# Kernel tuning notes

Hardware: AMD Instinct MI355X
Metric: run time of the kernel (lower is better)

Reference implementation:

```python
import jax, jax.numpy as jnp
import numpy as np

N_NODES = 100000
N_EDGES = 1600000
D = 128


def setup_inputs() -> dict:
    key = jax.random.key(0)
    ks = jax.random.split(key, 6)
    x = jax.random.normal(ks[0], (N_NODES, D), dtype=jnp.float32)
    src = jax.random.randint(ks[1], (N_EDGES,), 0, N_NODES, dtype=jnp.int32)
    dst = jax.random.randint(ks[2], (N_EDGES,), 0, N_NODES, dtype=jnp.int32)
    # Xavier-ish small weights
    W1 = jax.random.normal(ks[3], (D, D), dtype=jnp.float32) * 0.05
    W2 = jax.random.normal(ks[4], (D, D), dtype=jnp.float32) * 0.05
    b1 = jnp.zeros((D,), dtype=jnp.float32)
    b2 = jnp.zeros((D,), dtype=jnp.float32)
    prelu_a = jnp.full((1,), 0.25, dtype=jnp.float32)  # nn.PReLU default, shared across layers
    return {"x": x, "src": src, "dst": dst, "W1": W1, "b1": b1, "W2": W2, "b2": b2, "prelu_a": prelu_a}


def reference(x, src, dst, W1, b1, W2, b2, prelu_a):
    N = x.shape[0]
    # DGL GraphConv norm='left': scale source features by 1/clamp(out_degree, 1)
    deg = jax.ops.segment_sum(jnp.ones(src.shape, x.dtype), src, num_segments=N)
    inv_outdeg = (1.0 / jnp.maximum(deg, 1.0))[:, None]  # [N,1]

    def layer(h, W, b):
        h = h * inv_outdeg                                   # left-normalize sources
        agg = jax.ops.segment_sum(h[src], dst, num_segments=N)  # SpMM: sum messages at dst
        z = agg @ W + b                                      # dense transform (aggregate-first since in==out feats)
        return jnp.where(z >= 0, z, prelu_a * z)             # shared PReLU

    z = layer(x, W1, b1)
    z = layer(z, W2, b2)
    return z
```

## Files before the change

### kernel.cpp

```cpp
#include <hip/hip_runtime.h>

#define D 128
#define CAP 64
#define PADR 136

#define BSHIFT 9
#define NCH 512
#define BSTRIDE_LOG 14

typedef short short8 __attribute__((ext_vector_type(8)));
typedef float floatx4 __attribute__((ext_vector_type(4)));

static __device__ __forceinline__ unsigned short f2bf(float f) {
    unsigned int u = __float_as_uint(f);
    u += 0x7fffu + ((u >> 16) & 1u);
    return (unsigned short)(u >> 16);
}
static __device__ __forceinline__ unsigned int pack2bf(float a, float b) {
    return (unsigned int)f2bf(a) | ((unsigned int)f2bf(b) << 16);
}
static __device__ __forceinline__ int rd16(const unsigned int* __restrict__ pc, int v) {
    return (int)((pc[v >> 1] >> ((v & 1) * 16)) & 0xffffu);
}
static __device__ __forceinline__ void acc8(float* a, uint4 v) {
    a[0] += __uint_as_float(v.x << 16);  a[1] += __uint_as_float(v.x & 0xffff0000u);
    a[2] += __uint_as_float(v.y << 16);  a[3] += __uint_as_float(v.y & 0xffff0000u);
    a[4] += __uint_as_float(v.z << 16);  a[5] += __uint_as_float(v.z & 0xffff0000u);
    a[6] += __uint_as_float(v.w << 16);  a[7] += __uint_as_float(v.w & 0xffff0000u);
}

__global__ __launch_bounds__(512) void k_cnt(const int* __restrict__ src,
                                             const int* __restrict__ dst,
                                             unsigned int* __restrict__ gcd,
                                             unsigned int* __restrict__ gcs,
                                             int E, int cs, int nbuck) {
    __shared__ unsigned int hd[512], hs[512];
    int b = blockIdx.x, t = threadIdx.x;
    hd[t] = 0; hs[t] = 0;
    __syncthreads();
    int lo = b * cs, hi = lo + cs;
    if (hi > E) hi = E;
    for (int e = lo + t; e < hi; e += 512) {
        atomicAdd(&hd[(unsigned)dst[e] >> BSHIFT], 1u);
        atomicAdd(&hs[(unsigned)src[e] >> BSHIFT], 1u);
    }
    __syncthreads();
    for (int k = t; k < nbuck; k += 512) {
        gcd[(size_t)b * nbuck + k] = hd[k];
        gcs[(size_t)b * nbuck + k] = hs[k];
    }
}

__global__ __launch_bounds__(NCH) void k_pfx1(unsigned int* __restrict__ gcd,
                                              unsigned int* __restrict__ gcs,
                                              unsigned int* __restrict__ btd,
                                              unsigned int* __restrict__ bts, int nbuck) {
    __shared__ unsigned int sa[NCH], sb[NCH];
    int b = blockIdx.x, t = threadIdx.x;
    unsigned int* g  = (b < nbuck) ? gcd : gcs;
    unsigned int* bt = (b < nbuck) ? btd : bts;
    int k = (b < nbuck) ? b : (b - nbuck);
    unsigned int v = g[(size_t)t * nbuck + k];
    sa[t] = v;
    unsigned int* A = sa; unsigned int* B = sb;
    for (int off = 1; off < NCH; off <<= 1) {
        __syncthreads();
        B[t] = A[t] + ((t >= off) ? A[t - off] : 0u);
        unsigned int* tmp = A; A = B; B = tmp;
    }
    __syncthreads();
    unsigned int incl = A[t];
    g[(size_t)t * nbuck + k] = incl - v;
    if (t == NCH - 1) bt[k] = incl;
}

__global__ __launch_bounds__(512) void k_scat(const int* __restrict__ src, const int* __restrict__ dst,
                                              const unsigned int* __restrict__ gcd,
                                              const unsigned int* __restrict__ gcs,
                                              unsigned int* __restrict__ bdata,
                                              unsigned int* __restrict__ sdata,
                                              int E, int cs, int nbuck) {
    __shared__ unsigned int curd[512], curs[512];
    int b = blockIdx.x, t = threadIdx.x;
    for (int k = t; k < nbuck; k += 512) {
        curd[k] = ((unsigned int)k << BSTRIDE_LOG) + gcd[(size_t)b * nbuck + k];
        curs[k] = ((unsigned int)k << BSTRIDE_LOG) + gcs[(size_t)b * nbuck + k];
    }
    __syncthreads();
    int lo = b * cs, hi = lo + cs;
    if (hi > E) hi = E;
    for (int e = lo + t; e < hi; e += 512) {
        int s = src[e];
        int d = dst[e];
        unsigned int kd = (unsigned)d >> BSHIFT;
        unsigned int p = atomicAdd(&curd[kd], 1u);
        if (p < ((kd + 1u) << BSTRIDE_LOG))
            bdata[p] = ((unsigned int)(d & ((1 << BSHIFT) - 1)) << 17) | (unsigned int)s;
        unsigned int ks = (unsigned)s >> BSHIFT;
        unsigned int p2 = atomicAdd(&curs[ks], 1u);
        if (p2 < ((ks + 1u) << BSTRIDE_LOG))
            sdata[p2] = (unsigned int)(s & ((1 << BSHIFT) - 1));
    }
}

__global__ __launch_bounds__(256) void k_sdeg(const unsigned int* __restrict__ sdata,
                                              const unsigned int* __restrict__ bts,
                                              unsigned int* __restrict__ pcnt_out, int n) {
    __shared__ unsigned int cnt[1 << BSHIFT];
    int b = blockIdx.x;
    for (int k = threadIdx.x; k < (1 << BSHIFT); k += 256) cnt[k] = 0;
    __syncthreads();
    int lo = b << BSTRIDE_LOG;
    int c = (int)bts[b];
    if (c > (1 << BSTRIDE_LOG)) c = 1 << BSTRIDE_LOG;
    for (int i = threadIdx.x; i < c; i += 256)
        atomicAdd(&cnt[sdata[lo + i]], 1u);
    __syncthreads();
    int base = b << BSHIFT;
    for (int tt = threadIdx.x; tt < (1 << (BSHIFT - 1)); tt += 256) {
        int node0 = base + tt * 2;
        if (node0 < n) {
            unsigned int c0 = cnt[tt * 2];
            unsigned int c1 = cnt[tt * 2 + 1];
            pcnt_out[(base >> 1) + tt] = (c0 & 0xffffu) | (c1 << 16);
        }
    }
}

__global__ __launch_bounds__(256) void k_csrprep(
    const unsigned int* __restrict__ bdata, const unsigned int* __restrict__ btot,
    unsigned int* __restrict__ pcnt_in, int* __restrict__ esrc,
    const float* __restrict__ x, const unsigned int* __restrict__ pcnt_out,
    float* __restrict__ inv, uint2* __restrict__ xb2, int total4,
    const float* __restrict__ W1, const float* __restrict__ W2,
    unsigned short* __restrict__ WT1, unsigned short* __restrict__ WT2,
    uint4* __restrict__ z0, uint4* __restrict__ z1,
    int n, int nbuck) {
    __shared__ unsigned int lcnt[1 << BSHIFT];
    int b = blockIdx.x;

    if (b < nbuck) {
        int base = b << BSHIFT;
        for (int k = threadIdx.x; k < (1 << BSHIFT); k += 256) lcnt[k] = 0;
        __syncthreads();
        int lo = b << BSTRIDE_LOG;
        int cnt = (int)btot[b];
        if (cnt > (1 << BSTRIDE_LOG)) cnt = 1 << BSTRIDE_LOG;
        for (int i = threadIdx.x; i < cnt; i += 256) {
            unsigned int e = bdata[lo + i];
            int s = (int)(e & 0x1FFFFu);
            int dl = (int)(e >> 17);
            unsigned int p = atomicAdd(&lcnt[dl], 1u);
            if (p < CAP) esrc[((size_t)(base + dl) << 6) + p] = s;
        }
        __syncthreads();
        for (int nn = threadIdx.x; nn < (1 << BSHIFT); nn += 256) {
            int node = base + nn;
            if (node < n) {
                int c = (int)lcnt[nn];
                if (c > CAP) c = CAP;
                int cp = (c + 7) & ~7;
                for (int p = c; p < cp; p++)
                    esrc[((size_t)node << 6) + p] = n;
            }
        }
        for (int tt = threadIdx.x; tt < (1 << (BSHIFT - 1)); tt += 256) {
            int node0 = base + tt * 2;
            if (node0 < n) {
                unsigned int c0 = lcnt[tt * 2];
                unsigned int c1 = lcnt[tt * 2 + 1];
                pcnt_in[(base >> 1) + tt] = (c0 & 0xffffu) | (c1 << 16);
            }
        }
        return;
    }

    int bb = b - nbuck;
    int nb4 = (total4 + 255) >> 8;
    if (bb >= nb4 + 128) {
        if (threadIdx.x < 16) z0[threadIdx.x] = (uint4){0u, 0u, 0u, 0u};
        else if (threadIdx.x < 32) z1[threadIdx.x - 16] = (uint4){0u, 0u, 0u, 0u};
        return;
    }
    if (bb >= nb4) {
        int wb = bb - nb4;
        const float* W = (wb < 64) ? W1 : W2;
        unsigned short* WT = (wb < 64) ? WT1 : WT2;
        int idx = (wb & 63) * 256 + threadIdx.x;
        int k = idx >> 7, nn = idx & 127;
        WT[nn * 128 + k] = f2bf(W[idx]);
        return;
    }
    int i = bb * 256 + threadIdx.x;
    if (i >= total4) return;
    int row = i >> 5;
    int d = rd16(pcnt_out, row);
    float s = 1.0f / (float)(d > 1 ? d : 1);
    if ((i & 31) == 0) inv[row] = s;
    float4 v = ((const float4*)x)[i];
    uint2 o;
    o.x = pack2bf(v.x * s, v.y * s);
    o.y = pack2bf(v.z * s, v.w * s);
    xb2[i] = o;
}

template<bool OUTBF>
__global__ __launch_bounds__(256) void k_fused(
    const uint4* __restrict__ hb4, const unsigned int* __restrict__ pcnt_in,
    const int* __restrict__ esrc, const unsigned short* __restrict__ WT,
    const float* __restrict__ bias, const float* __restrict__ pa,
    const float* __restrict__ inv, void* __restrict__ outp, int n)
{
    __shared__ unsigned short sAgg[16 * PADR];
    int wv = threadIdx.x >> 6;
    int lane = threadIdx.x & 63;
    int q = lane >> 4;
    int f = lane & 15;
    int nb = blockIdx.x * 16;

    for (int ii = 0; ii < 4; ii += 2) {
        int nodeA = nb + wv * 4 + ii;
        int nodeB = nodeA + 1;
        int cA = (nodeA < n) ? rd16(pcnt_in, nodeA) : 0;
        int cB = (nodeB < n) ? rd16(pcnt_in, nodeB) : 0;
        if (cA > CAP) cA = CAP;
        if (cB > CAP) cB = CAP;
        cA = (cA + 7) & ~7;
        cB = (cB + 7) & ~7;
        const int* epA = esrc + ((size_t)nodeA << 6);
        const int* epB = esrc + ((size_t)nodeB << 6);
        float accA[8], accB[8];
#pragma unroll
        for (int j = 0; j < 8; j++) { accA[j] = 0.f; accB[j] = 0.f; }
        int mx = cA > cB ? cA : cB;
        for (int base = 0; base < mx; base += 8) {
            bool dA = base < cA, dB = base < cB;
            int2 eA, eB;
            uint4 vA0, vA1, vB0, vB1;
            if (dA) eA = *(const int2*)(epA + base + 2 * q);
            if (dB) eB = *(const int2*)(epB + base + 2 * q);
            if (dA) { vA0 = hb4[(size_t)eA.x * 16 + f]; vA1 = hb4[(size_t)eA.y * 16 + f]; }
            if (dB) { vB0 = hb4[(size_t)eB.x * 16 + f]; vB1 = hb4[(size_t)eB.y * 16 + f]; }
            if (dA) { acc8(accA, vA0); acc8(accA, vA1); }
            if (dB) { acc8(accB, vB0); acc8(accB, vB1); }
        }
#pragma unroll
        for (int j = 0; j < 8; j++) {
            accA[j] += __shfl_xor(accA[j], 16, 64);
            accA[j] += __shfl_xor(accA[j], 32, 64);
            accB[j] += __shfl_xor(accB[j], 16, 64);
            accB[j] += __shfl_xor(accB[j], 32, 64);
        }
        if (q == 0) {
            uint4 oA, oB;
            oA.x = pack2bf(accA[0], accA[1]); oA.y = pack2bf(accA[2], accA[3]);
            oA.z = pack2bf(accA[4], accA[5]); oA.w = pack2bf(accA[6], accA[7]);
            oB.x = pack2bf(accB[0], accB[1]); oB.y = pack2bf(accB[2], accB[3]);
            oB.z = pack2bf(accB[4], accB[5]); oB.w = pack2bf(accB[6], accB[7]);
            if (nodeA < n) *(uint4*)&sAgg[(wv * 4 + ii) * PADR + f * 8] = oA;
            if (nodeB < n) *(uint4*)&sAgg[(wv * 4 + ii + 1) * PADR + f * 8] = oB;
        }
    }
    __syncthreads();

    int m = lane & 15;
    short8 a0 = *(const short8*)&sAgg[m * PADR +   0 + q * 8];
    short8 a1 = *(const short8*)&sAgg[m * PADR +  32 + q * 8];
    short8 a2 = *(const short8*)&sAgg[m * PADR +  64 + q * 8];
    short8 a3 = *(const short8*)&sAgg[m * PADR +  96 + q * 8];

    float alpha = pa[0];
    float* outf = (float*)outp;
    unsigned short* outb = (unsigned short*)outp;

    float invr[4];
    if (OUTBF) {
#pragma unroll
        for (int r = 0; r < 4; r++) {
            int row = nb + q * 4 + r;
            invr[r] = (row < n) ? inv[row] : 1.f;
        }
    }

#pragma unroll
    for (int tt = 0; tt < 2; tt++) {
        int t = wv * 2 + tt;
        int col = t * 16 + m;
        const short8* Bp = (const short8*)(WT + (size_t)col * 128 + q * 8);
        floatx4 acc = {0.f, 0.f, 0.f, 0.f};
        acc = __builtin_amdgcn_mfma_f32_16x16x32_bf16(a0, Bp[0],  acc, 0, 0, 0);
        acc = __builtin_amdgcn_mfma_f32_16x16x32_bf16(a1, Bp[4],  acc, 0, 0, 0);
        acc = __builtin_amdgcn_mfma_f32_16x16x32_bf16(a2, Bp[8],  acc, 0, 0, 0);
        acc = __builtin_amdgcn_mfma_f32_16x16x32_bf16(a3, Bp[12], acc, 0, 0, 0);
        float bb = bias[col];
#pragma unroll
        for (int r = 0; r < 4; r++) {
            int row = nb + q * 4 + r;
            if (row < n) {
                float z = acc[r] + bb;
                z = (z >= 0.f) ? z : alpha * z;
                if (OUTBF)
                    outb[(size_t)row * 128 + col] = f2bf(z * invr[r]);
                else
                    __builtin_nontemporal_store(z, &outf[(size_t)row * 128 + col]);
            }
        }
    }
}

__global__ __launch_bounds__(256) void k_gather(
    const uint4* __restrict__ hb4, const unsigned int* __restrict__ pcnt_in,
    const int* __restrict__ esrc, uint4* __restrict__ aggb4, int n)
{
    int lane = threadIdx.x & 63;
    int node = blockIdx.x * 4 + (threadIdx.x >> 6);
    if (node >= n) return;
    int q = lane >> 4, f = lane & 15;
    int cnt = rd16(pcnt_in, node);
    if (cnt > CAP) cnt = CAP;
    cnt = (cnt + 7) & ~7;
    const int* ep = esrc + ((size_t)node << 6);

    float acc[8];
#pragma unroll
    for (int j = 0; j < 8; j++) acc[j] = 0.f;

    for (int base = 0; base < cnt; base += 8) {
        int2 e = *(const int2*)(ep + base + 2 * q);
        uint4 v0 = hb4[(size_t)e.x * 16 + f];
        uint4 v1 = hb4[(size_t)e.y * 16 + f];
        acc8(acc, v0);
        acc8(acc, v1);
    }
#pragma unroll
    for (int j = 0; j < 8; j++) {
        acc[j] += __shfl_xor(acc[j], 16, 64);
        acc[j] += __shfl_xor(acc[j], 32, 64);
    }
    if (q == 0) {
        uint4 o;
        o.x = pack2bf(acc[0], acc[1]);
        o.y = pack2bf(acc[2], acc[3]);
        o.z = pack2bf(acc[4], acc[5]);
        o.w = pack2bf(acc[6], acc[7]);
        aggb4[(size_t)node * 16 + f] = o;
    }
}

__global__ __launch_bounds__(256) void k_gemm(
    const unsigned short* __restrict__ A, const unsigned short* __restrict__ WT,
    const float* __restrict__ bias, const float* __restrict__ pa,
    float* __restrict__ outf, int n)
{
    int lane = threadIdx.x & 63;
    int wv = threadIdx.x >> 6;
    int m = lane & 15, q = lane >> 4;
    int mbase = blockIdx.x * 64 + wv * 16;
    int arow = mbase + m;
    if (arow > n - 1) arow = n - 1;

    const short8* Ap = (const short8*)(A + (size_t)arow * 128 + q * 8);
    short8 a0 = Ap[0], a1 = Ap[4], a2 = Ap[8], a3 = Ap[12];

    float alpha = pa[0];
#pragma unroll
    for (int t = 0; t < 8; t++) {
        int col = t * 16 + m;
        const short8* Bp = (const short8*)(WT + (size_t)col * 128 + q * 8);
        floatx4 acc = {0.f, 0.f, 0.f, 0.f};
        acc = __builtin_amdgcn_mfma_f32_16x16x32_bf16(a0, Bp[0],  acc, 0, 0, 0);
        acc = __builtin_amdgcn_mfma_f32_16x16x32_bf16(a1, Bp[4],  acc, 0, 0, 0);
        acc = __builtin_amdgcn_mfma_f32_16x16x32_bf16(a2, Bp[8],  acc, 0, 0, 0);
        acc = __builtin_amdgcn_mfma_f32_16x16x32_bf16(a3, Bp[12], acc, 0, 0, 0);
        float bb = bias[col];
#pragma unroll
        for (int r = 0; r < 4; r++) {
            int row = mbase + q * 4 + r;
            if (row < n) {
                float z = acc[r] + bb;
                z = (z >= 0.f) ? z : alpha * z;
                outf[(size_t)row * 128 + col] = z;
            }
        }
    }
}

extern "C" void kernel_launch(void* const* d_in, const int* in_sizes, int n_in,
                              void* d_out, int out_size, void* d_ws, size_t ws_size,
                              hipStream_t stream) {
    const float* x   = (const float*)d_in[0];
    const int* src   = (const int*)d_in[1];
    const int* dst   = (const int*)d_in[2];
    const float* W1  = (const float*)d_in[3];
    const float* b1  = (const float*)d_in[4];
    const float* W2  = (const float*)d_in[5];
    const float* b2  = (const float*)d_in[6];
    const float* pa  = (const float*)d_in[7];
    float* out = (float*)d_out;

    const int N = in_sizes[0] / D;
    const int E = in_sizes[1];

    char* ws = (char*)d_ws;
    size_t off = 0;
    unsigned short* buf0 = (unsigned short*)(ws + off); off += (size_t)(N + 1) * D * 2;
    unsigned short* buf1 = (unsigned short*)(ws + off); off += (size_t)(N + 1) * D * 2;
    const size_t pc_words = (size_t)((N + 1) / 2);
    unsigned int* pcnt_out = (unsigned int*)(ws + off); off += pc_words * 4;
    unsigned int* pcnt_in  = (unsigned int*)(ws + off); off += pc_words * 4;
    float* inv   = (float*)(ws + off); off += (size_t)N * sizeof(float);
    unsigned short* WT1 = (unsigned short*)(ws + off); off += 128 * 128 * 2;
    unsigned short* WT2 = (unsigned short*)(ws + off); off += 128 * 128 * 2;
    size_t off_esrc = off;
    size_t need_big = off_esrc + (size_t)N * CAP * sizeof(int);
    bool big = (ws_size >= need_big);

    int* esrc = big ? (int*)(ws + off_esrc) : (int*)d_out;

    const int nbuck = (N + (1 << BSHIFT) - 1) >> BSHIFT;
    unsigned int* bdata = (unsigned int*)buf1;
    unsigned int* gcd   = bdata + ((size_t)nbuck << BSTRIDE_LOG);
    unsigned int* gcs   = gcd + (size_t)NCH * nbuck;
    unsigned int* btd   = gcs + (size_t)NCH * nbuck;
    unsigned int* bts   = btd + nbuck;
    unsigned int* sdata = (unsigned int*)buf0;

    const int cs = (E + NCH - 1) / NCH;
    const int total4 = N * (D / 4);
    uint4* z0 = (uint4*)(buf0 + (size_t)N * D);
    uint4* z1 = (uint4*)(buf1 + (size_t)N * D);

    k_cnt <<<NCH, 512, 0, stream>>>(src, dst, gcd, gcs, E, cs, nbuck);
    k_pfx1<<<2 * nbuck, NCH, 0, stream>>>(gcd, gcs, btd, bts, nbuck);
    k_scat<<<NCH, 512, 0, stream>>>(src, dst, gcd, gcs, bdata, sdata, E, cs, nbuck);
    k_sdeg<<<nbuck, 256, 0, stream>>>(sdata, bts, pcnt_out, N);

    const int nb4 = (total4 + 255) / 256;
    const int NBC = nbuck + nb4 + 128 + 1;
    k_csrprep<<<NBC, 256, 0, stream>>>(bdata, btd, pcnt_in, esrc,
                                       x, pcnt_out, inv, (uint2*)buf0, total4,
                                       W1, W2, WT1, WT2, z0, z1, N, nbuck);

    const int NBF = (N + 15) / 16;

    k_fused<true><<<NBF, 256, 0, stream>>>((const uint4*)buf0, pcnt_in, esrc, WT1, b1, pa, inv,
                                           (void*)buf1, N);

    if (big) {
        k_fused<false><<<NBF, 256, 0, stream>>>((const uint4*)buf1, pcnt_in, esrc, WT2, b2, pa, inv,
                                                (void*)out, N);
    } else {
        const int NBG = (N + 3) / 4;
        const int NBM = (N + 63) / 64;
        k_gather<<<NBG, 256, 0, stream>>>((const uint4*)buf1, pcnt_in, esrc, (uint4*)buf0, N);
        k_gemm<<<NBM, 256, 0, stream>>>(buf0, WT2, b2, pa, out, N);
    }
}
```

Before: 336.3 us.

## Sort destination nodes by padded in-degree class to balance SpMM waves

Builds a permutation of destination nodes grouped by padded in-degree class (a counting sort over 9 classes), using per-bucket histograms, a single-block prefix scan and a scatter kernel. The fused aggregate+GEMM kernels then process nodes in permuted order, so the paired nodes in each wavefront have similar edge counts and less time is lost to divergent loop trip counts. This adds two extra launches, including a serial scan, plus an indirection for row indices and scattered output writes.

```diff
diff --git a/kernel.cpp b/kernel.cpp
--- a/kernel.cpp
+++ b/kernel.cpp
@@ -130,6 +130,7 @@
 __global__ __launch_bounds__(256) void k_csrprep(
     const unsigned int* __restrict__ bdata, const unsigned int* __restrict__ btot,
     unsigned int* __restrict__ pcnt_in, int* __restrict__ esrc,
+    unsigned int* __restrict__ gclass,
     const float* __restrict__ x, const unsigned int* __restrict__ pcnt_out,
     float* __restrict__ inv, uint2* __restrict__ xb2, int total4,
     const float* __restrict__ W1, const float* __restrict__ W2,
@@ -137,11 +138,13 @@
     uint4* __restrict__ z0, uint4* __restrict__ z1,
     int n, int nbuck) {
     __shared__ unsigned int lcnt[1 << BSHIFT];
+    __shared__ unsigned int clh[9];
     int b = blockIdx.x;
 
     if (b < nbuck) {
         int base = b << BSHIFT;
         for (int k = threadIdx.x; k < (1 << BSHIFT); k += 256) lcnt[k] = 0;
+        if (threadIdx.x < 9) clh[threadIdx.x] = 0;
         __syncthreads();
         int lo = b << BSTRIDE_LOG;
         int cnt = (int)btot[b];
@@ -160,6 +163,7 @@
                 int c = (int)lcnt[nn];
                 if (c > CAP) c = CAP;
                 int cp = (c + 7) & ~7;
+                atomicAdd(&clh[cp >> 3], 1u);
                 for (int p = c; p < cp; p++)
                     esrc[((size_t)node << 6) + p] = n;
             }
@@ -172,6 +176,8 @@
                 pcnt_in[(base >> 1) + tt] = (c0 & 0xffffu) | (c1 << 16);
             }
         }
+        __syncthreads();
+        if (threadIdx.x < 9) gclass[b * 9 + threadIdx.x] = clh[threadIdx.x];
         return;
     }
 
@@ -204,10 +210,56 @@
     xb2[i] = o;
 }
 
+__global__ __launch_bounds__(64) void k_pscan(const unsigned int* __restrict__ gclass,
+                                              unsigned int* __restrict__ offCB, int nbuck) {
+    __shared__ unsigned int tot[9];
+    __shared__ unsigned int cls0[9];
+    int t = threadIdx.x;
+    if (t < 9) {
+        unsigned int run = 0;
+        for (int b = 0; b < nbuck; b++) {
+            offCB[(size_t)t * nbuck + b] = run;
+            run += gclass[b * 9 + t];
+        }
+        tot[t] = run;
+    }
+    __syncthreads();
+    if (t == 0) {
+        unsigned int run = 0;
+        for (int c = 0; c < 9; c++) { cls0[c] = run; run += tot[c]; }
+    }
+    __syncthreads();
+    if (t < 9) {
+        unsigned int add = cls0[t];
+        for (int b = 0; b < nbuck; b++) offCB[(size_t)t * nbuck + b] += add;
+    }
+}
+
+__global__ __launch_bounds__(256) void k_pwrite(const unsigned int* __restrict__ pcnt_in,
+                                                const unsigned int* __restrict__ offCB,
+                                                int* __restrict__ perm, int n, int nbuck) {
+    __shared__ unsigned int cur[9];
+    int b = blockIdx.x;
+    if (threadIdx.x < 9) cur[threadIdx.x] = offCB[(size_t)threadIdx.x * nbuck + b];
+    __syncthreads();
+    int base = b << BSHIFT;
+    for (int nn = threadIdx.x; nn < (1 << BSHIFT); nn += 256) {
+        int node = base + nn;
+        if (node < n) {
+            int c = rd16(pcnt_in, node);
+            if (c > CAP) c = CAP;
+            int cls = ((c + 7) & ~7) >> 3;
+            unsigned int p = atomicAdd(&cur[cls], 1u);
+            perm[p] = node;
+        }
+    }
+}
+
 template<bool OUTBF>
 __global__ __launch_bounds__(256) void k_fused(
     const uint4* __restrict__ hb4, const unsigned int* __restrict__ pcnt_in,
-    const int* __restrict__ esrc, const unsigned short* __restrict__ WT,
+    const int* __restrict__ esrc, const int* __restrict__ perm,
+    const unsigned short* __restrict__ WT,
     const float* __restrict__ bias, const float* __restrict__ pa,
     const float* __restrict__ inv, void* __restrict__ outp, int n)
 {
@@ -219,10 +271,12 @@
     int nb = blockIdx.x * 16;
 
     for (int ii = 0; ii < 4; ii += 2) {
-        int nodeA = nb + wv * 4 + ii;
-        int nodeB = nodeA + 1;
-        int cA = (nodeA < n) ? rd16(pcnt_in, nodeA) : 0;
-        int cB = (nodeB < n) ? rd16(pcnt_in, nodeB) : 0;
+        int slotA = nb + wv * 4 + ii;
+        int slotB = slotA + 1;
+        int nodeA = (slotA < n) ? perm[slotA] : 0;
+        int nodeB = (slotB < n) ? perm[slotB] : 0;
+        int cA = (slotA < n) ? rd16(pcnt_in, nodeA) : 0;
+        int cB = (slotB < n) ? rd16(pcnt_in, nodeB) : 0;
         if (cA > CAP) cA = CAP;
         if (cB > CAP) cB = CAP;
         cA = (cA + 7) & ~7;
@@ -257,8 +311,8 @@
             oA.z = pack2bf(accA[4], accA[5]); oA.w = pack2bf(accA[6], accA[7]);
             oB.x = pack2bf(accB[0], accB[1]); oB.y = pack2bf(accB[2], accB[3]);
             oB.z = pack2bf(accB[4], accB[5]); oB.w = pack2bf(accB[6], accB[7]);
-            if (nodeA < n) *(uint4*)&sAgg[(wv * 4 + ii) * PADR + f * 8] = oA;
-            if (nodeB < n) *(uint4*)&sAgg[(wv * 4 + ii + 1) * PADR + f * 8] = oB;
+            if (slotA < n) *(uint4*)&sAgg[(wv * 4 + ii) * PADR + f * 8] = oA;
+            if (slotB < n) *(uint4*)&sAgg[(wv * 4 + ii + 1) * PADR + f * 8] = oB;
         }
     }
     __syncthreads();
@@ -273,13 +327,13 @@
     float* outf = (float*)outp;
     unsigned short* outb = (unsigned short*)outp;
 
+    int rows[4];
     float invr[4];
-    if (OUTBF) {
-#pragma unroll
-        for (int r = 0; r < 4; r++) {
-            int row = nb + q * 4 + r;
-            invr[r] = (row < n) ? inv[row] : 1.f;
-        }
+#pragma unroll
+    for (int r = 0; r < 4; r++) {
+        int slot = nb + q * 4 + r;
+        rows[r] = (slot < n) ? perm[slot] : -1;
+        if (OUTBF) invr[r] = (rows[r] >= 0) ? inv[rows[r]] : 1.f;
     }
 
 #pragma unroll
@@ -295,8 +349,8 @@
         float bb = bias[col];
 #pragma unroll
         for (int r = 0; r < 4; r++) {
-            int row = nb + q * 4 + r;
-            if (row < n) {
+            int row = rows[r];
+            if (row >= 0) {
                 float z = acc[r] + bb;
                 z = (z >= 0.f) ? z : alpha * z;
                 if (OUTBF)
@@ -411,13 +465,16 @@
     float* inv   = (float*)(ws + off); off += (size_t)N * sizeof(float);
     unsigned short* WT1 = (unsigned short*)(ws + off); off += 128 * 128 * 2;
     unsigned short* WT2 = (unsigned short*)(ws + off); off += 128 * 128 * 2;
+    const int nbuck = (N + (1 << BSHIFT) - 1) >> BSHIFT;
+    unsigned int* gclass = (unsigned int*)(ws + off); off += (size_t)nbuck * 9 * 4;
+    unsigned int* offCB  = (unsigned int*)(ws + off); off += (size_t)nbuck * 9 * 4;
+    int* perm = (int*)(ws + off); off += (size_t)(N + 16) * 4;
     size_t off_esrc = off;
     size_t need_big = off_esrc + (size_t)N * CAP * sizeof(int);
     bool big = (ws_size >= need_big);
 
     int* esrc = big ? (int*)(ws + off_esrc) : (int*)d_out;
 
-    const int nbuck = (N + (1 << BSHIFT) - 1) >> BSHIFT;
     unsigned int* bdata = (unsigned int*)buf1;
     unsigned int* gcd   = bdata + ((size_t)nbuck << BSTRIDE_LOG);
     unsigned int* gcs   = gcd + (size_t)NCH * nbuck;
@@ -437,17 +494,20 @@
 
     const int nb4 = (total4 + 255) / 256;
     const int NBC = nbuck + nb4 + 128 + 1;
-    k_csrprep<<<NBC, 256, 0, stream>>>(bdata, btd, pcnt_in, esrc,
+    k_csrprep<<<NBC, 256, 0, stream>>>(bdata, btd, pcnt_in, esrc, gclass,
                                        x, pcnt_out, inv, (uint2*)buf0, total4,
                                        W1, W2, WT1, WT2, z0, z1, N, nbuck);
 
+    k_pscan <<<1, 64, 0, stream>>>(gclass, offCB, nbuck);
+    k_pwrite<<<nbuck, 256, 0, stream>>>(pcnt_in, offCB, perm, N, nbuck);
+
     const int NBF = (N + 15) / 16;
 
-    k_fused<true><<<NBF, 256, 0, stream>>>((const uint4*)buf0, pcnt_in, esrc, WT1, b1, pa, inv,
+    k_fused<true><<<NBF, 256, 0, stream>>>((const uint4*)buf0, pcnt_in, esrc, perm, WT1, b1, pa, inv,
                                            (void*)buf1, N);
 
     if (big) {
-        k_fused<false><<<NBF, 256, 0, stream>>>((const uint4*)buf1, pcnt_in, esrc, WT2, b2, pa, inv,
+        k_fused<false><<<NBF, 256, 0, stream>>>((const uint4*)buf1, pcnt_in, esrc, perm, WT2, b2, pa, inv,
                                                 (void*)out, N);
     } else {
         const int NBG = (N + 3) / 4;
```

Result: slower. 393.4 us (+17.0%).

## Fuse out-degree counting into x-scaling blocks and drop separate degree kernel

Applied to the files above, without the earlier changes.

Removes the k_sdeg launch. Each source bucket block now counts out-degrees in shared memory and immediately normalizes and converts its 512 rows of x to bf16, writing inv as well. Source-local indices are stored as 16-bit values in a region after the bucket tables, which halves that scatter traffic and frees buf0. The cost is that x scaling now runs on only ~196 blocks instead of thousands, so that work gets less parallelism.

```diff
diff --git a/kernel.cpp b/kernel.cpp
--- a/kernel.cpp
+++ b/kernel.cpp
@@ -78,7 +78,7 @@
                                               const unsigned int* __restrict__ gcd,
                                               const unsigned int* __restrict__ gcs,
                                               unsigned int* __restrict__ bdata,
-                                              unsigned int* __restrict__ sdata,
+                                              unsigned short* __restrict__ sdata,
                                               int E, int cs, int nbuck) {
     __shared__ unsigned int curd[512], curs[512];
     int b = blockIdx.x, t = threadIdx.x;
@@ -99,54 +99,65 @@
         unsigned int ks = (unsigned)s >> BSHIFT;
         unsigned int p2 = atomicAdd(&curs[ks], 1u);
         if (p2 < ((ks + 1u) << BSTRIDE_LOG))
-            sdata[p2] = (unsigned int)(s & ((1 << BSHIFT) - 1));
-    }
-}
-
-__global__ __launch_bounds__(256) void k_sdeg(const unsigned int* __restrict__ sdata,
-                                              const unsigned int* __restrict__ bts,
-                                              unsigned int* __restrict__ pcnt_out, int n) {
-    __shared__ unsigned int cnt[1 << BSHIFT];
-    int b = blockIdx.x;
-    for (int k = threadIdx.x; k < (1 << BSHIFT); k += 256) cnt[k] = 0;
-    __syncthreads();
-    int lo = b << BSTRIDE_LOG;
-    int c = (int)bts[b];
-    if (c > (1 << BSTRIDE_LOG)) c = 1 << BSTRIDE_LOG;
-    for (int i = threadIdx.x; i < c; i += 256)
-        atomicAdd(&cnt[sdata[lo + i]], 1u);
-    __syncthreads();
-    int base = b << BSHIFT;
-    for (int tt = threadIdx.x; tt < (1 << (BSHIFT - 1)); tt += 256) {
-        int node0 = base + tt * 2;
-        if (node0 < n) {
-            unsigned int c0 = cnt[tt * 2];
-            unsigned int c1 = cnt[tt * 2 + 1];
-            pcnt_out[(base >> 1) + tt] = (c0 & 0xffffu) | (c1 << 16);
-        }
-    }
-}
-
-__global__ __launch_bounds__(256) void k_csrprep(
-    const unsigned int* __restrict__ bdata, const unsigned int* __restrict__ btot,
+            sdata[p2] = (unsigned short)(s & ((1 << BSHIFT) - 1));
+    }
+}
+
+__global__ __launch_bounds__(256) void k_post(
+    const unsigned int* __restrict__ bdata, const unsigned short* __restrict__ sdata,
+    const unsigned int* __restrict__ btd, const unsigned int* __restrict__ bts,
     unsigned int* __restrict__ pcnt_in, int* __restrict__ esrc,
-    const float* __restrict__ x, const unsigned int* __restrict__ pcnt_out,
-    float* __restrict__ inv, uint2* __restrict__ xb2, int total4,
+    const float* __restrict__ x, float* __restrict__ inv, uint2* __restrict__ xb2,
     const float* __restrict__ W1, const float* __restrict__ W2,
     unsigned short* __restrict__ WT1, unsigned short* __restrict__ WT2,
     uint4* __restrict__ z0, uint4* __restrict__ z1,
     int n, int nbuck) {
     __shared__ unsigned int lcnt[1 << BSHIFT];
     int b = blockIdx.x;
+    int t = threadIdx.x;
 
     if (b < nbuck) {
-        int base = b << BSHIFT;
-        for (int k = threadIdx.x; k < (1 << BSHIFT); k += 256) lcnt[k] = 0;
+        for (int k = t; k < (1 << BSHIFT); k += 256) lcnt[k] = 0;
         __syncthreads();
         int lo = b << BSTRIDE_LOG;
-        int cnt = (int)btot[b];
+        int c = (int)bts[b];
+        if (c > (1 << BSTRIDE_LOG)) c = 1 << BSTRIDE_LOG;
+        for (int i = t; i < c; i += 256)
+            atomicAdd(&lcnt[sdata[lo + i]], 1u);
+        __syncthreads();
+        int base = b << BSHIFT;
+        for (int i = t; i < (1 << BSHIFT); i += 256) {
+            int node = base + i;
+            if (node < n) {
+                int dg = (int)lcnt[i];
+                inv[node] = 1.0f / (float)(dg > 1 ? dg : 1);
+            }
+        }
+        const int tot = (1 << BSHIFT) * 32;
+        for (int i = t; i < tot; i += 256) {
+            int r = i >> 5;
+            int node = base + r;
+            if (node >= n) continue;
+            int dg = (int)lcnt[r];
+            float s = 1.0f / (float)(dg > 1 ? dg : 1);
+            float4 v = ((const float4*)x)[(size_t)node * 32 + (i & 31)];
+            uint2 o;
+            o.x = pack2bf(v.x * s, v.y * s);
+            o.y = pack2bf(v.z * s, v.w * s);
+            xb2[(size_t)node * 32 + (i & 31)] = o;
+        }
+        return;
+    }
+
+    if (b < 2 * nbuck) {
+        int bb = b - nbuck;
+        int base = bb << BSHIFT;
+        for (int k = t; k < (1 << BSHIFT); k += 256) lcnt[k] = 0;
+        __syncthreads();
+        int lo = bb << BSTRIDE_LOG;
+        int cnt = (int)btd[bb];
         if (cnt > (1 << BSTRIDE_LOG)) cnt = 1 << BSTRIDE_LOG;
-        for (int i = threadIdx.x; i < cnt; i += 256) {
+        for (int i = t; i < cnt; i += 256) {
             unsigned int e = bdata[lo + i];
             int s = (int)(e & 0x1FFFFu);
             int dl = (int)(e >> 17);
@@ -154,7 +165,7 @@
             if (p < CAP) esrc[((size_t)(base + dl) << 6) + p] = s;
         }
         __syncthreads();
-        for (int nn = threadIdx.x; nn < (1 << BSHIFT); nn += 256) {
+        for (int nn = t; nn < (1 << BSHIFT); nn += 256) {
             int node = base + nn;
             if (node < n) {
                 int c = (int)lcnt[nn];
@@ -164,7 +175,7 @@
                     esrc[((size_t)node << 6) + p] = n;
             }
         }
-        for (int tt = threadIdx.x; tt < (1 << (BSHIFT - 1)); tt += 256) {
+        for (int tt = t; tt < (1 << (BSHIFT - 1)); tt += 256) {
             int node0 = base + tt * 2;
             if (node0 < n) {
                 unsigned int c0 = lcnt[tt * 2];
@@ -175,33 +186,17 @@
         return;
     }
 
-    int bb = b - nbuck;
-    int nb4 = (total4 + 255) >> 8;
-    if (bb >= nb4 + 128) {
-        if (threadIdx.x < 16) z0[threadIdx.x] = (uint4){0u, 0u, 0u, 0u};
-        else if (threadIdx.x < 32) z1[threadIdx.x - 16] = (uint4){0u, 0u, 0u, 0u};
+    int wb = b - 2 * nbuck;
+    if (wb >= 128) {
+        if (t < 16) z0[t] = (uint4){0u, 0u, 0u, 0u};
+        else if (t < 32) z1[t - 16] = (uint4){0u, 0u, 0u, 0u};
         return;
     }
-    if (bb >= nb4) {
-        int wb = bb - nb4;
-        const float* W = (wb < 64) ? W1 : W2;
-        unsigned short* WT = (wb < 64) ? WT1 : WT2;
-        int idx = (wb & 63) * 256 + threadIdx.x;
-        int k = idx >> 7, nn = idx & 127;
-        WT[nn * 128 + k] = f2bf(W[idx]);
-        return;
-    }
-    int i = bb * 256 + threadIdx.x;
-    if (i >= total4) return;
-    int row = i >> 5;
-    int d = rd16(pcnt_out, row);
-    float s = 1.0f / (float)(d > 1 ? d : 1);
-    if ((i & 31) == 0) inv[row] = s;
-    float4 v = ((const float4*)x)[i];
-    uint2 o;
-    o.x = pack2bf(v.x * s, v.y * s);
-    o.y = pack2bf(v.z * s, v.w * s);
-    xb2[i] = o;
+    const float* W = (wb < 64) ? W1 : W2;
+    unsigned short* WT = (wb < 64) ? WT1 : WT2;
+    int idx = (wb & 63) * 256 + t;
+    int k = idx >> 7, nn = idx & 127;
+    WT[nn * 128 + k] = f2bf(W[idx]);
 }
 
 template<bool OUTBF>
@@ -406,7 +401,6 @@
     unsigned short* buf0 = (unsigned short*)(ws + off); off += (size_t)(N + 1) * D * 2;
     unsigned short* buf1 = (unsigned short*)(ws + off); off += (size_t)(N + 1) * D * 2;
     const size_t pc_words = (size_t)((N + 1) / 2);
-    unsigned int* pcnt_out = (unsigned int*)(ws + off); off += pc_words * 4;
     unsigned int* pcnt_in  = (unsigned int*)(ws + off); off += pc_words * 4;
     float* inv   = (float*)(ws + off); off += (size_t)N * sizeof(float);
     unsigned short* WT1 = (unsigned short*)(ws + off); off += 128 * 128 * 2;
@@ -423,23 +417,20 @@
     unsigned int* gcs   = gcd + (size_t)NCH * nbuck;
     unsigned int* btd   = gcs + (size_t)NCH * nbuck;
     unsigned int* bts   = btd + nbuck;
-    unsigned int* sdata = (unsigned int*)buf0;
+    unsigned short* sdata = (unsigned short*)(bts + nbuck);
 
     const int cs = (E + NCH - 1) / NCH;
-    const int total4 = N * (D / 4);
     uint4* z0 = (uint4*)(buf0 + (size_t)N * D);
     uint4* z1 = (uint4*)(buf1 + (size_t)N * D);
 
     k_cnt <<<NCH, 512, 0, stream>>>(src, dst, gcd, gcs, E, cs, nbuck);
     k_pfx1<<<2 * nbuck, NCH, 0, stream>>>(gcd, gcs, btd, bts, nbuck);
     k_scat<<<NCH, 512, 0, stream>>>(src, dst, gcd, gcs, bdata, sdata, E, cs, nbuck);
-    k_sdeg<<<nbuck, 256, 0, stream>>>(sdata, bts, pcnt_out, N);
-
-    const int nb4 = (total4 + 255) / 256;
-    const int NBC = nbuck + nb4 + 128 + 1;
-    k_csrprep<<<NBC, 256, 0, stream>>>(bdata, btd, pcnt_in, esrc,
-                                       x, pcnt_out, inv, (uint2*)buf0, total4,
-                                       W1, W2, WT1, WT2, z0, z1, N, nbuck);
+
+    const int NBP = 2 * nbuck + 128 + 1;
+    k_post<<<NBP, 256, 0, stream>>>(bdata, sdata, btd, bts, pcnt_in, esrc,
+                                    x, inv, (uint2*)buf0, W1, W2, WT1, WT2, z0, z1,
+                                    N, nbuck);
 
     const int NBF = (N + 15) / 16;
 
```

New measurement: 367.0 us. +9.1%, slower.
